# Kernel optimization log

Hardware: AMD Instinct MI355X
Metric: run time of the kernel (lower is better)

Reference implementation:

```python
import jax, jax.numpy as jnp
import numpy as np

N_ATOMS = 200000
N_EDGES = 400000  # directed edges, paired: rev(2i)=2i+1
ATOM_DIM = 133
BOND_DIM = 14
HIDDEN = 256
NUM_GRAPHS = 8000


def setup_inputs() -> dict:
    key = jax.random.key(0)
    ks = jax.random.split(key, 10)
    V = jax.random.normal(ks[0], (N_ATOMS, ATOM_DIM), dtype=jnp.float32)
    E = jax.random.normal(ks[1], (N_EDGES, BOND_DIM), dtype=jnp.float32)
    weight = jnp.ones((N_EDGES,), dtype=jnp.float32)
    # paired directed edges: (s,d) then (d,s)
    half = N_EDGES // 2
    s = jax.random.randint(ks[2], (half,), 0, N_ATOMS, dtype=jnp.int32)
    d = jax.random.randint(ks[3], (half,), 0, N_ATOMS, dtype=jnp.int32)
    src = jnp.stack([s, d], axis=1).reshape(-1)
    dst = jnp.stack([d, s], axis=1).reshape(-1)
    edge_index = jnp.stack([src, dst], axis=0)
    rev_edge_index = jnp.bitwise_xor(jnp.arange(N_EDGES, dtype=jnp.int32), 1)
    atom_batch = jnp.sort(jax.random.randint(ks[4], (N_ATOMS,), 0, NUM_GRAPHS, dtype=jnp.int32))
    scale = 0.02
    W_i = jax.random.normal(ks[5], (HIDDEN, ATOM_DIM + BOND_DIM), dtype=jnp.float32) * scale
    W_h = jax.random.normal(ks[6], (HIDDEN, HIDDEN), dtype=jnp.float32) * scale
    W_o_w = jax.random.normal(ks[7], (HIDDEN, ATOM_DIM + HIDDEN), dtype=jnp.float32) * scale
    W_o_b = jnp.zeros((HIDDEN,), dtype=jnp.float32)
    return {"V": V, "E": E, "weight": weight, "W_i": W_i, "W_h": W_h,
            "W_o_w": W_o_w, "W_o_b": W_o_b, "edge_index": edge_index,
            "rev_edge_index": rev_edge_index, "atom_batch": atom_batch,
            "num_graphs": NUM_GRAPHS}


def reference(V, E, weight, W_i, W_h, W_o_w, W_o_b, edge_index, rev_edge_index, atom_batch, num_graphs):
    n_atoms = V.shape[0]
    src, dst = edge_index[0], edge_index[1]
    relu = jax.nn.relu
    # initial edge hidden state: h0 = relu(W_i [V[src]; E])
    inp = jnp.concatenate([V[src], E], axis=1)              # [E, atom+bond]
    h0 = relu(inp @ W_i.T)                                   # [E, H]
    h = h0
    T = 3
    for _ in range(T):
        # weighted scatter of edge messages into destination atoms
        m_to_atom = jax.ops.segment_sum(h * weight[:, None], dst, num_segments=n_atoms)  # [N, H]
        # gather back to source atom of each edge, subtract reverse-edge contribution
        m = m_to_atom[src] - weight[rev_edge_index][:, None] * h[rev_edge_index]          # [E, H]
        h = relu(m @ W_h.T + h0)
    m_final = jax.ops.segment_sum(h, dst, num_segments=n_atoms)                           # [N, H]
    h_atom = relu(jnp.concatenate([V, m_final], axis=1) @ W_o_w.T + W_o_b)                # [N, H]
    mol_vecs = jax.ops.segment_sum(h_atom, atom_batch, num_segments=num_graphs)           # [G, H]
    return h_atom, atom_batch, mol_vecs, h
```

## Files before the change

kernel.cpp:

```cpp
#include <hip/hip_runtime.h>

#define N_ATOMS   200000
#define N_EDGESC  400000
#define HID       256
#define NGRAPH    8000

typedef __attribute__((ext_vector_type(8))) short bf16x8;
typedef __attribute__((ext_vector_type(8))) unsigned short u16x8;
typedef __attribute__((ext_vector_type(4))) unsigned short u16x4;
typedef __attribute__((ext_vector_type(4))) float f32x4;

__device__ inline ushort bfc(float x) {
    union { float f; unsigned u; } u; u.f = x;
    unsigned r = u.u + 0x7fff + ((u.u >> 16) & 1);
    return (ushort)(r >> 16);
}
__device__ inline float b2f(ushort u) {
    union { unsigned u; float f; } x; x.u = ((unsigned)u) << 16; return x.f;
}

__global__ void prep_weights(const float* __restrict__ Wi, const float* __restrict__ Wh,
                             const float* __restrict__ Wo, ushort* __restrict__ Wib,
                             ushort* __restrict__ Whb, ushort* __restrict__ Wob) {
    int i = blockIdx.x * 256 + threadIdx.x;
    if (i < 256 * 256) Whb[i] = bfc(Wh[i]);
    if (i < 256 * 192) {
        int t = i / 192, k = i % 192;
        float v = 0.f;
        if (k < 133) v = Wi[t * 147 + k];
        else if (k >= 136 && k < 150) v = Wi[t * 147 + 133 + (k - 136)];
        Wib[i] = bfc(v);
    }
    if (i < 256 * 448) {
        int t = i / 448, k = i % 448;
        float v = 0.f;
        if (k < 133) v = Wo[t * 389 + k];
        else if (k >= 136 && k < 392) v = Wo[t * 389 + 133 + (k - 136)];
        Wob[i] = bfc(v);
    }
}

__global__ void count_kernel(const int* __restrict__ dst, int* __restrict__ cnt, int n) {
    int i = blockIdx.x * blockDim.x + threadIdx.x;
    if (i < n) atomicAdd(&cnt[dst[i]], 1);
}

__global__ void scan_kernel(const int* deg, int* offs, int* cursor, int n) {
    __shared__ int ssum[1024];
    __shared__ int s_base;
    int tid = threadIdx.x;
    if (tid == 0) s_base = 0;
    __syncthreads();
    const int TPT = 8;
    const int TILE = 1024 * TPT;
    for (int start = 0; start < n; start += TILE) {
        int base_i = start + tid * TPT;
        int v[TPT];
        int s = 0;
#pragma unroll
        for (int j = 0; j < TPT; j++) {
            int i = base_i + j;
            v[j] = (i < n) ? deg[i] : 0;
            s += v[j];
        }
        ssum[tid] = s;
        __syncthreads();
        for (int off = 1; off < 1024; off <<= 1) {
            int x = (tid >= off) ? ssum[tid - off] : 0;
            __syncthreads();
            ssum[tid] += x;
            __syncthreads();
        }
        int thr_excl = ssum[tid] - s;
        int tile_total = ssum[1023];
        int run = s_base + thr_excl;
#pragma unroll
        for (int j = 0; j < TPT; j++) {
            int i = base_i + j;
            if (i < n) { offs[i] = run; cursor[i] = run; run += v[j]; }
        }
        __syncthreads();
        if (tid == 0) s_base += tile_total;
        __syncthreads();
    }
    if (tid == 0) offs[n] = s_base;
}

__global__ void fill_kernel(const int* __restrict__ dst, int* __restrict__ cursor,
                            int* __restrict__ eids, int n) {
    int i = blockIdx.x * blockDim.x + threadIdx.x;
    if (i < n) {
        int p = atomicAdd(&cursor[dst[i]], 1);
        eids[p] = i;
    }
}

__global__ __launch_bounds__(256) void h0_mfma(const float* __restrict__ V,
                                               const float* __restrict__ E,
                                               const ushort* __restrict__ Wib,
                                               const int* __restrict__ src,
                                               ushort* __restrict__ h0b) {
    __shared__ char lds[64 * 384];
    int t = threadIdx.x;
    int e0 = blockIdx.x * 64;
#pragma unroll
    for (int i = 0; i < 6; i++) {
        int c = t + i * 256;
        int e = c / 24, kc = c % 24;
        int ge = e0 + e;
        int s = src[ge];
        int k0 = kc * 8;
        bf16x8 v;
#pragma unroll
        for (int j = 0; j < 8; j++) {
            int k = k0 + j;
            float x;
            if (k < 133) x = V[(size_t)s * 133 + k];
            else if (k < 136) x = 0.f;
            else if (k < 150) x = E[(size_t)ge * 14 + (k - 136)];
            else x = 0.f;
            v[j] = (short)bfc(x);
        }
        int addr = (e * 384 + k0 * 2) ^ ((e & 7) << 4);
        *(bf16x8*)(lds + addr) = v;
    }
    __syncthreads();
    int lane = t & 63, w = t >> 6;
    int n0 = w * 64;
    int lq = lane >> 4, lr = lane & 15;
    f32x4 acc[4][4];
#pragma unroll
    for (int mt = 0; mt < 4; mt++)
#pragma unroll
        for (int nt = 0; nt < 4; nt++) acc[mt][nt] = {0.f, 0.f, 0.f, 0.f};
    for (int ks = 0; ks < 6; ks++) {
        int kk = ks * 32 + lq * 8;
        bf16x8 af[4], bfr[4];
#pragma unroll
        for (int mt = 0; mt < 4; mt++) {
            int row = mt * 16 + lr;
            int addr = (row * 384 + kk * 2) ^ ((row & 7) << 4);
            af[mt] = *(const bf16x8*)(lds + addr);
        }
#pragma unroll
        for (int nt = 0; nt < 4; nt++) {
            int col = n0 + nt * 16 + lr;
            bfr[nt] = *(const bf16x8*)&Wib[col * 192 + kk];
        }
#pragma unroll
        for (int mt = 0; mt < 4; mt++)
#pragma unroll
            for (int nt = 0; nt < 4; nt++)
                acc[mt][nt] = __builtin_amdgcn_mfma_f32_16x16x32_bf16(af[mt], bfr[nt], acc[mt][nt], 0, 0, 0);
    }
#pragma unroll
    for (int mt = 0; mt < 4; mt++)
#pragma unroll
        for (int nt = 0; nt < 4; nt++)
#pragma unroll
            for (int j = 0; j < 4; j++) {
                int row = mt * 16 + lq * 4 + j;
                int col = n0 + nt * 16 + lr;
                size_t idx = (size_t)(e0 + row) * HID + col;
                float v = acc[mt][nt][j];
                h0b[idx] = bfc(v > 0.f ? v : 0.f);
            }
}

template <int FINAL>
__global__ __launch_bounds__(256) void mp_mfma(const ushort* __restrict__ mta_b,
                                               const ushort* __restrict__ h0b,
                                               const ushort* __restrict__ Whb,
                                               const float* __restrict__ weight,
                                               const int* __restrict__ src,
                                               const int* __restrict__ rev,
                                               const ushort* __restrict__ hr_b,
                                               ushort* __restrict__ hw_b,
                                               float* __restrict__ hw_f) {
    __shared__ char lds[64 * 512];
    int t = threadIdx.x;
    int e0 = blockIdx.x * 64;
    int e = t >> 2, q = t & 3;
    int ge = e0 + e;
    int s = src[ge], r = rev[ge];
    float wr = weight[r];
    const u16x8* mrow = (const u16x8*)&mta_b[(size_t)s * HID];
    const u16x8* hrow = (const u16x8*)&hr_b[(size_t)r * HID];
    u16x8 ma[8], ha[8];
#pragma unroll
    for (int i = 0; i < 8; i++) ma[i] = mrow[q + i * 4];
#pragma unroll
    for (int i = 0; i < 8; i++) ha[i] = hrow[q + i * 4];
#pragma unroll
    for (int i = 0; i < 8; i++) {
        int chunk = q + i * 4;
        u16x8 v;
#pragma unroll
        for (int j = 0; j < 8; j++)
            v[j] = bfc(b2f(ma[i][j]) - wr * b2f(ha[i][j]));
        int addr = (e * 512 + chunk * 16) ^ ((e & 7) << 4);
        *(u16x8*)(lds + addr) = v;
    }
    __syncthreads();
    int lane = t & 63, w = t >> 6;
    int n0 = w * 64;
    int lq = lane >> 4, lr = lane & 15;
    f32x4 acc[4][4];
#pragma unroll
    for (int mt = 0; mt < 4; mt++)
#pragma unroll
        for (int nt = 0; nt < 4; nt++) acc[mt][nt] = {0.f, 0.f, 0.f, 0.f};
    for (int ks = 0; ks < 8; ks++) {
        int kk = ks * 32 + lq * 8;
        bf16x8 af[4], bfr[4];
#pragma unroll
        for (int mt = 0; mt < 4; mt++) {
            int row = mt * 16 + lr;
            int addr = (row * 512 + kk * 2) ^ ((row & 7) << 4);
            af[mt] = *(const bf16x8*)(lds + addr);
        }
#pragma unroll
        for (int nt = 0; nt < 4; nt++) {
            int col = n0 + nt * 16 + lr;
            bfr[nt] = *(const bf16x8*)&Whb[col * 256 + kk];
        }
#pragma unroll
        for (int mt = 0; mt < 4; mt++)
#pragma unroll
            for (int nt = 0; nt < 4; nt++)
                acc[mt][nt] = __builtin_amdgcn_mfma_f32_16x16x32_bf16(af[mt], bfr[nt], acc[mt][nt], 0, 0, 0);
    }
#pragma unroll
    for (int mt = 0; mt < 4; mt++)
#pragma unroll
        for (int nt = 0; nt < 4; nt++)
#pragma unroll
            for (int j = 0; j < 4; j++) {
                int row = mt * 16 + lq * 4 + j;
                int col = n0 + nt * 16 + lr;
                size_t idx = (size_t)(e0 + row) * HID + col;
                float v = acc[mt][nt][j] + b2f(h0b[idx]);
                v = v > 0.f ? v : 0.f;
                if (FINAL) hw_f[idx] = v;
                else       hw_b[idx] = bfc(v);
            }
}

__global__ __launch_bounds__(256) void out_mfma(const float* __restrict__ V,
                                                const ushort* __restrict__ mfin,
                                                const ushort* __restrict__ Wob,
                                                const float* __restrict__ bias,
                                                float* __restrict__ h_atom) {
    __shared__ char lds[64 * 896];
    int t = threadIdx.x;
    int a0 = blockIdx.x * 64;
#pragma unroll
    for (int i = 0; i < 14; i++) {
        int c = t + i * 256;
        int e = c / 56, kc = c % 56;
        int a = a0 + e;
        int k0 = kc * 8;
        u16x8 v;
#pragma unroll
        for (int j = 0; j < 8; j++) {
            int k = k0 + j;
            ushort x;
            if (k < 133) x = bfc(V[(size_t)a * 133 + k]);
            else if (k < 136) x = 0;
            else if (k < 392) x = mfin[(size_t)a * HID + (k - 136)];
            else x = 0;
            v[j] = x;
        }
        int addr = (e * 896 + k0 * 2) ^ ((e & 7) << 4);
        *(u16x8*)(lds + addr) = v;
    }
    __syncthreads();
    int lane = t & 63, w = t >> 6;
    int n0 = w * 64;
    int lq = lane >> 4, lr = lane & 15;
    f32x4 acc[4][4];
#pragma unroll
    for (int mt = 0; mt < 4; mt++)
#pragma unroll
        for (int nt = 0; nt < 4; nt++) acc[mt][nt] = {0.f, 0.f, 0.f, 0.f};
    for (int ks = 0; ks < 14; ks++) {
        int kk = ks * 32 + lq * 8;
        bf16x8 af[4], bfr[4];
#pragma unroll
        for (int mt = 0; mt < 4; mt++) {
            int row = mt * 16 + lr;
            int addr = (row * 896 + kk * 2) ^ ((row & 7) << 4);
            af[mt] = *(const bf16x8*)(lds + addr);
        }
#pragma unroll
        for (int nt = 0; nt < 4; nt++) {
            int col = n0 + nt * 16 + lr;
            bfr[nt] = *(const bf16x8*)&Wob[col * 448 + kk];
        }
#pragma unroll
        for (int mt = 0; mt < 4; mt++)
#pragma unroll
            for (int nt = 0; nt < 4; nt++)
                acc[mt][nt] = __builtin_amdgcn_mfma_f32_16x16x32_bf16(af[mt], bfr[nt], acc[mt][nt], 0, 0, 0);
    }
#pragma unroll
    for (int mt = 0; mt < 4; mt++)
#pragma unroll
        for (int nt = 0; nt < 4; nt++)
#pragma unroll
            for (int j = 0; j < 4; j++) {
                int row = mt * 16 + lq * 4 + j;
                int col = n0 + nt * 16 + lr;
                size_t idx = (size_t)(a0 + row) * HID + col;
                float v = acc[mt][nt][j] + bias[col];
                h_atom[idx] = v > 0.f ? v : 0.f;
            }
}

__global__ void seg_reduce_b(const ushort* __restrict__ h, const float* __restrict__ weight,
                             const int* __restrict__ offs, const int* __restrict__ eids,
                             ushort* __restrict__ out) {
    int t = threadIdx.x;
    int a = blockIdx.x * 4 + (t >> 6);
    int c = t & 63;
    int lo = offs[a], hi = offs[a + 1];
    float acc0 = 0.f, acc1 = 0.f, acc2 = 0.f, acc3 = 0.f;
    for (int i = lo; i < hi; i++) {
        int e = eids[i];
        float w = weight[e];
        u16x4 x = ((const u16x4*)&h[(size_t)e * HID])[c];
        acc0 += w * b2f(x[0]); acc1 += w * b2f(x[1]);
        acc2 += w * b2f(x[2]); acc3 += w * b2f(x[3]);
    }
    u16x4 o; o[0] = bfc(acc0); o[1] = bfc(acc1); o[2] = bfc(acc2); o[3] = bfc(acc3);
    ((u16x4*)&out[(size_t)a * HID])[c] = o;
}

__global__ void seg_reduce_f(const float* __restrict__ h,
                             const int* __restrict__ offs, const int* __restrict__ eids,
                             ushort* __restrict__ out) {
    int t = threadIdx.x;
    int a = blockIdx.x * 4 + (t >> 6);
    int c = t & 63;
    int lo = offs[a], hi = offs[a + 1];
    float4 acc = {0.f, 0.f, 0.f, 0.f};
    for (int i = lo; i < hi; i++) {
        int e = eids[i];
        float4 x = ((const float4*)&h[(size_t)e * HID])[c];
        acc.x += x.x; acc.y += x.y; acc.z += x.z; acc.w += x.w;
    }
    u16x4 o; o[0] = bfc(acc.x); o[1] = bfc(acc.y); o[2] = bfc(acc.z); o[3] = bfc(acc.w);
    ((u16x4*)&out[(size_t)a * HID])[c] = o;
}

__global__ void mol_kernel(const float* __restrict__ h_atom, const int* __restrict__ batch,
                           float* __restrict__ mol) {
    int g = blockIdx.x;
    int t = threadIdx.x;
    __shared__ int s_lo, s_hi;
    if (t == 0) {
        int lo = 0, hi = N_ATOMS;
        while (lo < hi) { int mid = (lo + hi) >> 1; if (batch[mid] < g) lo = mid + 1; else hi = mid; }
        s_lo = lo;
        int lo2 = lo, hi2 = N_ATOMS;
        while (lo2 < hi2) { int mid = (lo2 + hi2) >> 1; if (batch[mid] < g + 1) lo2 = mid + 1; else hi2 = mid; }
        s_hi = lo2;
    }
    __syncthreads();
    float acc = 0.f;
    for (int a = s_lo; a < s_hi; a++) acc += h_atom[(size_t)a * HID + t];
    mol[(size_t)g * HID + t] = acc;
}

__global__ void batchf_kernel(const int* __restrict__ batch, float* __restrict__ outb, int n) {
    int i = blockIdx.x * blockDim.x + threadIdx.x;
    if (i < n) outb[i] = (float)batch[i];
}

extern "C" void kernel_launch(void* const* d_in, const int* in_sizes, int n_in,
                              void* d_out, int out_size, void* d_ws, size_t ws_size,
                              hipStream_t stream) {
    const float* V      = (const float*)d_in[0];
    const float* E      = (const float*)d_in[1];
    const float* weight = (const float*)d_in[2];
    const float* W_i    = (const float*)d_in[3];
    const float* W_h    = (const float*)d_in[4];
    const float* W_o    = (const float*)d_in[5];
    const float* W_b    = (const float*)d_in[6];
    const int*   eidx   = (const int*)d_in[7];
    const int*   src    = eidx;
    const int*   dst    = eidx + N_EDGESC;
    const int*   rev    = (const int*)d_in[8];
    const int*   batch  = (const int*)d_in[9];

    float* out     = (float*)d_out;
    float* o_hatom = out;
    float* o_batch = out + (size_t)51200000;
    float* o_mol   = out + (size_t)51400000;
    float* o_h     = out + (size_t)53448000;

    char* base = (char*)d_ws;
    ushort* h0b    = (ushort*)(base);
    ushort* h_b    = (ushort*)(base + 204800000ull);
    ushort* mta_b  = (ushort*)(base + 409600000ull);
    ushort* Whb    = (ushort*)(base + 512000000ull);
    ushort* Wib    = (ushort*)(base + 512131072ull);
    ushort* Wob    = (ushort*)(base + 512229376ull);
    int*    offs   = (int*)(base + 512458752ull);
    int*    cursor = (int*)(base + 513258768ull);
    int*    eids   = (int*)(base + 514058768ull);

    hipMemsetAsync(cursor, 0, N_ATOMS * sizeof(int), stream);

    prep_weights<<<448, 256, 0, stream>>>(W_i, W_h, W_o, Wib, Whb, Wob);
    count_kernel<<<(N_EDGESC + 255) / 256, 256, 0, stream>>>(dst, cursor, N_EDGESC);
    scan_kernel<<<1, 1024, 0, stream>>>(cursor, offs, cursor, N_ATOMS);
    fill_kernel<<<(N_EDGESC + 255) / 256, 256, 0, stream>>>(dst, cursor, eids, N_EDGESC);

    h0_mfma<<<N_EDGESC / 64, 256, 0, stream>>>(V, E, Wib, src, h0b);

    seg_reduce_b<<<N_ATOMS / 4, 256, 0, stream>>>(h0b, weight, offs, eids, mta_b);
    mp_mfma<0><<<N_EDGESC / 64, 256, 0, stream>>>(mta_b, h0b, Whb, weight, src, rev, h0b, h_b, nullptr);

    seg_reduce_b<<<N_ATOMS / 4, 256, 0, stream>>>(h_b, weight, offs, eids, mta_b);
    mp_mfma<0><<<N_EDGESC / 64, 256, 0, stream>>>(mta_b, h0b, Whb, weight, src, rev, h_b, h_b, nullptr);

    seg_reduce_b<<<N_ATOMS / 4, 256, 0, stream>>>(h_b, weight, offs, eids, mta_b);
    mp_mfma<1><<<N_EDGESC / 64, 256, 0, stream>>>(mta_b, h0b, Whb, weight, src, rev, h_b, nullptr, o_h);

    seg_reduce_f<<<N_ATOMS / 4, 256, 0, stream>>>(o_h, offs, eids, mta_b);
    out_mfma<<<N_ATOMS / 64, 256, 0, stream>>>(V, mta_b, Wob, W_b, o_hatom);
    mol_kernel<<<NGRAPH, 256, 0, stream>>>(o_hatom, batch, o_mol);
    batchf_kernel<<<(N_ATOMS + 255) / 256, 256, 0, stream>>>(batch, o_batch, N_ATOMS);
}
```

Before: 2.753 ms.

## Parallelize CSR scan, swap MFMA operands for vectorized stores, widen mp blocks

Replaces the single-block serial scan with a three-kernel parallel scan (block sums, top-level scan, finalize), which removes a long single-CU serial phase. Swaps the MFMA A/B operands so each lane holds four contiguous output channels, allowing packed bf16x4 or float4 epilogue stores instead of scalar 2-byte stores. Uses the hardware v_cvt_pk_bf16_f32 instruction for conversions. Changes mp_mfma to 512 threads with a 2x4 wave tiling, which halves per-wave accumulators but adds more waves per block. Adds deg/part workspace buffers.

```diff
diff --git a/kernel.cpp b/kernel.cpp
--- a/kernel.cpp
+++ b/kernel.cpp
@@ -6,8 +6,6 @@
 #define NGRAPH    8000
 
 typedef __attribute__((ext_vector_type(8))) short bf16x8;
-typedef __attribute__((ext_vector_type(8))) unsigned short u16x8;
-typedef __attribute__((ext_vector_type(4))) unsigned short u16x4;
 typedef __attribute__((ext_vector_type(4))) float f32x4;
 
 __device__ inline ushort bfc(float x) {
@@ -18,6 +16,15 @@
 __device__ inline float b2f(ushort u) {
     union { unsigned u; float f; } x; x.u = ((unsigned)u) << 16; return x.f;
 }
+__device__ inline float u2f(unsigned u) {
+    union { unsigned u; float f; } x; x.u = u; return x.f;
+}
+__device__ inline unsigned pk2(float a, float b) {
+    unsigned r;
+    asm volatile("v_cvt_pk_bf16_f32 %0, %1, %2" : "=v"(r) : "v"(a), "v"(b));
+    return r;
+}
+__device__ inline float relu(float v) { return v > 0.f ? v : 0.f; }
 
 __global__ void prep_weights(const float* __restrict__ Wi, const float* __restrict__ Wh,
                              const float* __restrict__ Wo, ushort* __restrict__ Wib,
@@ -45,45 +52,52 @@
     if (i < n) atomicAdd(&cnt[dst[i]], 1);
 }
 
-__global__ void scan_kernel(const int* deg, int* offs, int* cursor, int n) {
-    __shared__ int ssum[1024];
-    __shared__ int s_base;
-    int tid = threadIdx.x;
-    if (tid == 0) s_base = 0;
-    __syncthreads();
-    const int TPT = 8;
-    const int TILE = 1024 * TPT;
-    for (int start = 0; start < n; start += TILE) {
-        int base_i = start + tid * TPT;
-        int v[TPT];
-        int s = 0;
-#pragma unroll
-        for (int j = 0; j < TPT; j++) {
-            int i = base_i + j;
-            v[j] = (i < n) ? deg[i] : 0;
-            s += v[j];
-        }
-        ssum[tid] = s;
+__global__ void scan_part(const int* __restrict__ deg, int* __restrict__ part, int n) {
+    __shared__ int sm[256];
+    int t = threadIdx.x;
+    int i = blockIdx.x * 256 + t;
+    int v = (i < n) ? deg[i] : 0;
+    sm[t] = v; __syncthreads();
+    for (int off = 128; off > 0; off >>= 1) {
+        if (t < off) sm[t] += sm[t + off];
         __syncthreads();
-        for (int off = 1; off < 1024; off <<= 1) {
-            int x = (tid >= off) ? ssum[tid - off] : 0;
-            __syncthreads();
-            ssum[tid] += x;
-            __syncthreads();
-        }
-        int thr_excl = ssum[tid] - s;
-        int tile_total = ssum[1023];
-        int run = s_base + thr_excl;
-#pragma unroll
-        for (int j = 0; j < TPT; j++) {
-            int i = base_i + j;
-            if (i < n) { offs[i] = run; cursor[i] = run; run += v[j]; }
-        }
+    }
+    if (t == 0) part[blockIdx.x] = sm[0];
+}
+
+__global__ void scan_tops(int* __restrict__ part, int nb, int* __restrict__ offs) {
+    __shared__ int sm[1024];
+    int t = threadIdx.x;
+    int v = (t < nb) ? part[t] : 0;
+    sm[t] = v; __syncthreads();
+    for (int off = 1; off < 1024; off <<= 1) {
+        int x = (t >= off) ? sm[t - off] : 0;
         __syncthreads();
-        if (tid == 0) s_base += tile_total;
+        sm[t] += x;
         __syncthreads();
     }
-    if (tid == 0) offs[n] = s_base;
+    if (t < nb) part[t] = sm[t] - v;
+    if (t == 0) offs[N_ATOMS] = N_EDGESC;
+}
+
+__global__ void scan_fin(const int* __restrict__ deg, const int* __restrict__ part,
+                         int* __restrict__ offs, int* __restrict__ cursor, int n) {
+    __shared__ int sm[256];
+    int t = threadIdx.x;
+    int i = blockIdx.x * 256 + t;
+    int v = (i < n) ? deg[i] : 0;
+    sm[t] = v; __syncthreads();
+    for (int off = 1; off < 256; off <<= 1) {
+        int x = (t >= off) ? sm[t - off] : 0;
+        __syncthreads();
+        sm[t] += x;
+        __syncthreads();
+    }
+    if (i < n) {
+        int excl = sm[t] - v + part[blockIdx.x];
+        offs[i] = excl;
+        cursor[i] = excl;
+    }
 }
 
 __global__ void fill_kernel(const int* __restrict__ dst, int* __restrict__ cursor,
@@ -110,7 +124,7 @@
         int ge = e0 + e;
         int s = src[ge];
         int k0 = kc * 8;
-        bf16x8 v;
+        float xs[8];
 #pragma unroll
         for (int j = 0; j < 8; j++) {
             int k = k0 + j;
@@ -119,10 +133,13 @@
             else if (k < 136) x = 0.f;
             else if (k < 150) x = E[(size_t)ge * 14 + (k - 136)];
             else x = 0.f;
-            v[j] = (short)bfc(x);
-        }
+            xs[j] = x;
+        }
+        uint4 o;
+        o.x = pk2(xs[0], xs[1]); o.y = pk2(xs[2], xs[3]);
+        o.z = pk2(xs[4], xs[5]); o.w = pk2(xs[6], xs[7]);
         int addr = (e * 384 + k0 * 2) ^ ((e & 7) << 4);
-        *(bf16x8*)(lds + addr) = v;
+        *(uint4*)(lds + addr) = o;
     }
     __syncthreads();
     int lane = t & 63, w = t >> 6;
@@ -151,24 +168,23 @@
         for (int mt = 0; mt < 4; mt++)
 #pragma unroll
             for (int nt = 0; nt < 4; nt++)
-                acc[mt][nt] = __builtin_amdgcn_mfma_f32_16x16x32_bf16(af[mt], bfr[nt], acc[mt][nt], 0, 0, 0);
+                acc[mt][nt] = __builtin_amdgcn_mfma_f32_16x16x32_bf16(bfr[nt], af[mt], acc[mt][nt], 0, 0, 0);
     }
 #pragma unroll
     for (int mt = 0; mt < 4; mt++)
 #pragma unroll
-        for (int nt = 0; nt < 4; nt++)
-#pragma unroll
-            for (int j = 0; j < 4; j++) {
-                int row = mt * 16 + lq * 4 + j;
-                int col = n0 + nt * 16 + lr;
-                size_t idx = (size_t)(e0 + row) * HID + col;
-                float v = acc[mt][nt][j];
-                h0b[idx] = bfc(v > 0.f ? v : 0.f);
-            }
+        for (int nt = 0; nt < 4; nt++) {
+            int row = e0 + mt * 16 + lr;
+            int chan = n0 + nt * 16 + lq * 4;
+            float v0 = relu(acc[mt][nt][0]), v1 = relu(acc[mt][nt][1]);
+            float v2 = relu(acc[mt][nt][2]), v3 = relu(acc[mt][nt][3]);
+            uint2 o; o.x = pk2(v0, v1); o.y = pk2(v2, v3);
+            *(uint2*)&h0b[(size_t)row * HID + chan] = o;
+        }
 }
 
 template <int FINAL>
-__global__ __launch_bounds__(256) void mp_mfma(const ushort* __restrict__ mta_b,
+__global__ __launch_bounds__(512) void mp_mfma(const ushort* __restrict__ mta_b,
                                                const ushort* __restrict__ h0b,
                                                const ushort* __restrict__ Whb,
                                                const float* __restrict__ weight,
@@ -180,70 +196,93 @@
     __shared__ char lds[64 * 512];
     int t = threadIdx.x;
     int e0 = blockIdx.x * 64;
-    int e = t >> 2, q = t & 3;
+    int e = t >> 3, q = t & 7;
     int ge = e0 + e;
     int s = src[ge], r = rev[ge];
-    float wr = weight[r];
-    const u16x8* mrow = (const u16x8*)&mta_b[(size_t)s * HID];
-    const u16x8* hrow = (const u16x8*)&hr_b[(size_t)r * HID];
-    u16x8 ma[8], ha[8];
-#pragma unroll
-    for (int i = 0; i < 8; i++) ma[i] = mrow[q + i * 4];
-#pragma unroll
-    for (int i = 0; i < 8; i++) ha[i] = hrow[q + i * 4];
-#pragma unroll
-    for (int i = 0; i < 8; i++) {
-        int chunk = q + i * 4;
-        u16x8 v;
-#pragma unroll
-        for (int j = 0; j < 8; j++)
-            v[j] = bfc(b2f(ma[i][j]) - wr * b2f(ha[i][j]));
+    float nwr = -weight[r];
+    const uint4* mrow = (const uint4*)&mta_b[(size_t)s * HID];
+    const uint4* hrow = (const uint4*)&hr_b[(size_t)r * HID];
+    uint4 ma[4], ha[4];
+#pragma unroll
+    for (int i = 0; i < 4; i++) ma[i] = mrow[q + 8 * i];
+#pragma unroll
+    for (int i = 0; i < 4; i++) ha[i] = hrow[q + 8 * i];
+#pragma unroll
+    for (int i = 0; i < 4; i++) {
+        int chunk = q + 8 * i;
+        uint4 o;
+        {
+            unsigned mw = ma[i].x, hw = ha[i].x;
+            o.x = pk2(fmaf(nwr, u2f(hw << 16), u2f(mw << 16)),
+                      fmaf(nwr, u2f(hw & 0xffff0000u), u2f(mw & 0xffff0000u)));
+        }
+        {
+            unsigned mw = ma[i].y, hw = ha[i].y;
+            o.y = pk2(fmaf(nwr, u2f(hw << 16), u2f(mw << 16)),
+                      fmaf(nwr, u2f(hw & 0xffff0000u), u2f(mw & 0xffff0000u)));
+        }
+        {
+            unsigned mw = ma[i].z, hw = ha[i].z;
+            o.z = pk2(fmaf(nwr, u2f(hw << 16), u2f(mw << 16)),
+                      fmaf(nwr, u2f(hw & 0xffff0000u), u2f(mw & 0xffff0000u)));
+        }
+        {
+            unsigned mw = ma[i].w, hw = ha[i].w;
+            o.w = pk2(fmaf(nwr, u2f(hw << 16), u2f(mw << 16)),
+                      fmaf(nwr, u2f(hw & 0xffff0000u), u2f(mw & 0xffff0000u)));
+        }
         int addr = (e * 512 + chunk * 16) ^ ((e & 7) << 4);
-        *(u16x8*)(lds + addr) = v;
+        *(uint4*)(lds + addr) = o;
     }
     __syncthreads();
-    int lane = t & 63, w = t >> 6;
-    int n0 = w * 64;
+    int lane = t & 63, wid = t >> 6;
+    int wr = wid >> 2, wc = wid & 3;
     int lq = lane >> 4, lr = lane & 15;
-    f32x4 acc[4][4];
-#pragma unroll
-    for (int mt = 0; mt < 4; mt++)
+    f32x4 acc[2][4];
+#pragma unroll
+    for (int mt = 0; mt < 2; mt++)
 #pragma unroll
         for (int nt = 0; nt < 4; nt++) acc[mt][nt] = {0.f, 0.f, 0.f, 0.f};
     for (int ks = 0; ks < 8; ks++) {
         int kk = ks * 32 + lq * 8;
-        bf16x8 af[4], bfr[4];
-#pragma unroll
-        for (int mt = 0; mt < 4; mt++) {
-            int row = mt * 16 + lr;
+        bf16x8 af[2], bfr[4];
+#pragma unroll
+        for (int mt = 0; mt < 2; mt++) {
+            int row = wr * 32 + mt * 16 + lr;
             int addr = (row * 512 + kk * 2) ^ ((row & 7) << 4);
             af[mt] = *(const bf16x8*)(lds + addr);
         }
 #pragma unroll
         for (int nt = 0; nt < 4; nt++) {
-            int col = n0 + nt * 16 + lr;
+            int col = wc * 64 + nt * 16 + lr;
             bfr[nt] = *(const bf16x8*)&Whb[col * 256 + kk];
         }
 #pragma unroll
-        for (int mt = 0; mt < 4; mt++)
+        for (int mt = 0; mt < 2; mt++)
 #pragma unroll
             for (int nt = 0; nt < 4; nt++)
-                acc[mt][nt] = __builtin_amdgcn_mfma_f32_16x16x32_bf16(af[mt], bfr[nt], acc[mt][nt], 0, 0, 0);
-    }
-#pragma unroll
-    for (int mt = 0; mt < 4; mt++)
-#pragma unroll
-        for (int nt = 0; nt < 4; nt++)
-#pragma unroll
-            for (int j = 0; j < 4; j++) {
-                int row = mt * 16 + lq * 4 + j;
-                int col = n0 + nt * 16 + lr;
-                size_t idx = (size_t)(e0 + row) * HID + col;
-                float v = acc[mt][nt][j] + b2f(h0b[idx]);
-                v = v > 0.f ? v : 0.f;
-                if (FINAL) hw_f[idx] = v;
-                else       hw_b[idx] = bfc(v);
+                acc[mt][nt] = __builtin_amdgcn_mfma_f32_16x16x32_bf16(bfr[nt], af[mt], acc[mt][nt], 0, 0, 0);
+    }
+#pragma unroll
+    for (int mt = 0; mt < 2; mt++)
+#pragma unroll
+        for (int nt = 0; nt < 4; nt++) {
+            int row = e0 + wr * 32 + mt * 16 + lr;
+            int chan = wc * 64 + nt * 16 + lq * 4;
+            size_t idx = (size_t)row * HID + chan;
+            uint2 h0v = *(const uint2*)&h0b[idx];
+            float v0 = relu(acc[mt][nt][0] + u2f(h0v.x << 16));
+            float v1 = relu(acc[mt][nt][1] + u2f(h0v.x & 0xffff0000u));
+            float v2 = relu(acc[mt][nt][2] + u2f(h0v.y << 16));
+            float v3 = relu(acc[mt][nt][3] + u2f(h0v.y & 0xffff0000u));
+            if (FINAL) {
+                float4 o; o.x = v0; o.y = v1; o.z = v2; o.w = v3;
+                *(float4*)&hw_f[idx] = o;
+            } else {
+                uint2 o; o.x = pk2(v0, v1); o.y = pk2(v2, v3);
+                *(uint2*)&hw_b[idx] = o;
             }
+        }
 }
 
 __global__ __launch_bounds__(256) void out_mfma(const float* __restrict__ V,
@@ -260,24 +299,31 @@
         int e = c / 56, kc = c % 56;
         int a = a0 + e;
         int k0 = kc * 8;
-        u16x8 v;
+        float xs[8];
 #pragma unroll
         for (int j = 0; j < 8; j++) {
             int k = k0 + j;
-            ushort x;
-            if (k < 133) x = bfc(V[(size_t)a * 133 + k]);
-            else if (k < 136) x = 0;
-            else if (k < 392) x = mfin[(size_t)a * HID + (k - 136)];
-            else x = 0;
-            v[j] = x;
-        }
+            float x;
+            if (k < 133) x = V[(size_t)a * 133 + k];
+            else if (k < 136) x = 0.f;
+            else if (k < 392) x = b2f(mfin[(size_t)a * HID + (k - 136)]);
+            else x = 0.f;
+            xs[j] = x;
+        }
+        uint4 o;
+        o.x = pk2(xs[0], xs[1]); o.y = pk2(xs[2], xs[3]);
+        o.z = pk2(xs[4], xs[5]); o.w = pk2(xs[6], xs[7]);
         int addr = (e * 896 + k0 * 2) ^ ((e & 7) << 4);
-        *(u16x8*)(lds + addr) = v;
+        *(uint4*)(lds + addr) = o;
     }
     __syncthreads();
     int lane = t & 63, w = t >> 6;
     int n0 = w * 64;
     int lq = lane >> 4, lr = lane & 15;
+    float4 b4[4];
+#pragma unroll
+    for (int nt = 0; nt < 4; nt++)
+        b4[nt] = *(const float4*)&bias[n0 + nt * 16 + lq * 4];
     f32x4 acc[4][4];
 #pragma unroll
     for (int mt = 0; mt < 4; mt++)
@@ -301,20 +347,21 @@
         for (int mt = 0; mt < 4; mt++)
 #pragma unroll
             for (int nt = 0; nt < 4; nt++)
-                acc[mt][nt] = __builtin_amdgcn_mfma_f32_16x16x32_bf16(af[mt], bfr[nt], acc[mt][nt], 0, 0, 0);
+                acc[mt][nt] = __builtin_amdgcn_mfma_f32_16x16x32_bf16(bfr[nt], af[mt], acc[mt][nt], 0, 0, 0);
     }
 #pragma unroll
     for (int mt = 0; mt < 4; mt++)
 #pragma unroll
-        for (int nt = 0; nt < 4; nt++)
-#pragma unroll
-            for (int j = 0; j < 4; j++) {
-                int row = mt * 16 + lq * 4 + j;
-                int col = n0 + nt * 16 + lr;
-                size_t idx = (size_t)(a0 + row) * HID + col;
-                float v = acc[mt][nt][j] + bias[col];
-                h_atom[idx] = v > 0.f ? v : 0.f;
-            }
+        for (int nt = 0; nt < 4; nt++) {
+            int row = a0 + mt * 16 + lr;
+            int chan = n0 + nt * 16 + lq * 4;
+            float4 o;
+            o.x = relu(acc[mt][nt][0] + b4[nt].x);
+            o.y = relu(acc[mt][nt][1] + b4[nt].y);
+            o.z = relu(acc[mt][nt][2] + b4[nt].z);
+            o.w = relu(acc[mt][nt][3] + b4[nt].w);
+            *(float4*)&h_atom[(size_t)row * HID + chan] = o;
+        }
 }
 
 __global__ void seg_reduce_b(const ushort* __restrict__ h, const float* __restrict__ weight,
@@ -328,12 +375,12 @@
     for (int i = lo; i < hi; i++) {
         int e = eids[i];
         float w = weight[e];
-        u16x4 x = ((const u16x4*)&h[(size_t)e * HID])[c];
-        acc0 += w * b2f(x[0]); acc1 += w * b2f(x[1]);
-        acc2 += w * b2f(x[2]); acc3 += w * b2f(x[3]);
-    }
-    u16x4 o; o[0] = bfc(acc0); o[1] = bfc(acc1); o[2] = bfc(acc2); o[3] = bfc(acc3);
-    ((u16x4*)&out[(size_t)a * HID])[c] = o;
+        uint2 x = ((const uint2*)&h[(size_t)e * HID])[c];
+        acc0 += w * u2f(x.x << 16); acc1 += w * u2f(x.x & 0xffff0000u);
+        acc2 += w * u2f(x.y << 16); acc3 += w * u2f(x.y & 0xffff0000u);
+    }
+    uint2 o; o.x = pk2(acc0, acc1); o.y = pk2(acc2, acc3);
+    ((uint2*)&out[(size_t)a * HID])[c] = o;
 }
 
 __global__ void seg_reduce_f(const float* __restrict__ h,
@@ -349,8 +396,8 @@
         float4 x = ((const float4*)&h[(size_t)e * HID])[c];
         acc.x += x.x; acc.y += x.y; acc.z += x.z; acc.w += x.w;
     }
-    u16x4 o; o[0] = bfc(acc.x); o[1] = bfc(acc.y); o[2] = bfc(acc.z); o[3] = bfc(acc.w);
-    ((u16x4*)&out[(size_t)a * HID])[c] = o;
+    uint2 o; o.x = pk2(acc.x, acc.y); o.y = pk2(acc.z, acc.w);
+    ((uint2*)&out[(size_t)a * HID])[c] = o;
 }
 
 __global__ void mol_kernel(const float* __restrict__ h_atom, const int* __restrict__ batch,
@@ -409,24 +456,30 @@
     int*    offs   = (int*)(base + 512458752ull);
     int*    cursor = (int*)(base + 513258768ull);
     int*    eids   = (int*)(base + 514058768ull);
-
-    hipMemsetAsync(cursor, 0, N_ATOMS * sizeof(int), stream);
+    int*    deg    = (int*)(base + 515658768ull);
+    int*    part   = (int*)(base + 516458768ull);
+
+    const int NB = (N_ATOMS + 255) / 256;
+
+    hipMemsetAsync(deg, 0, N_ATOMS * sizeof(int), stream);
 
     prep_weights<<<448, 256, 0, stream>>>(W_i, W_h, W_o, Wib, Whb, Wob);
-    count_kernel<<<(N_EDGESC + 255) / 256, 256, 0, stream>>>(dst, cursor, N_EDGESC);
-    scan_kernel<<<1, 1024, 0, stream>>>(cursor, offs, cursor, N_ATOMS);
+    count_kernel<<<(N_EDGESC + 255) / 256, 256, 0, stream>>>(dst, deg, N_EDGESC);
+    scan_part<<<NB, 256, 0, stream>>>(deg, part, N_ATOMS);
+    scan_tops<<<1, 1024, 0, stream>>>(part, NB, offs);
+    scan_fin<<<NB, 256, 0, stream>>>(deg, part, offs, cursor, N_ATOMS);
     fill_kernel<<<(N_EDGESC + 255) / 256, 256, 0, stream>>>(dst, cursor, eids, N_EDGESC);
 
     h0_mfma<<<N_EDGESC / 64, 256, 0, stream>>>(V, E, Wib, src, h0b);
 
     seg_reduce_b<<<N_ATOMS / 4, 256, 0, stream>>>(h0b, weight, offs, eids, mta_b);
-    mp_mfma<0><<<N_EDGESC / 64, 256, 0, stream>>>(mta_b, h0b, Whb, weight, src, rev, h0b, h_b, nullptr);
+    mp_mfma<0><<<N_EDGESC / 64, 512, 0, stream>>>(mta_b, h0b, Whb, weight, src, rev, h0b, h_b, nullptr);
 
     seg_reduce_b<<<N_ATOMS / 4, 256, 0, stream>>>(h_b, weight, offs, eids, mta_b);
-    mp_mfma<0><<<N_EDGESC / 64, 256, 0, stream>>>(mta_b, h0b, Whb, weight, src, rev, h_b, h_b, nullptr);
+    mp_mfma<0><<<N_EDGESC / 64, 512, 0, stream>>>(mta_b, h0b, Whb, weight, src, rev, h_b, h_b, nullptr);
 
     seg_reduce_b<<<N_ATOMS / 4, 256, 0, stream>>>(h_b, weight, offs, eids, mta_b);
-    mp_mfma<1><<<N_EDGESC / 64, 256, 0, stream>>>(mta_b, h0b, Whb, weight, src, rev, h_b, nullptr, o_h);
+    mp_mfma<1><<<N_EDGESC / 64, 512, 0, stream>>>(mta_b, h0b, Whb, weight, src, rev, h_b, nullptr, o_h);
 
     seg_reduce_f<<<N_ATOMS / 4, 256, 0, stream>>>(o_h, offs, eids, mta_b);
     out_mfma<<<N_ATOMS / 64, 256, 0, stream>>>(V, mta_b, Wob, W_b, o_hatom);
```

After: 2.765 ms. About the same (+0.4%).
